# Optimization experiments

Hardware: AMD Instinct MI355X
Metric: run time of the kernel (lower is better)

The kernel has to match this reference:

```python
import jax, jax.numpy as jnp
import numpy as np

C = 512
G = 2  # num_groups in Normalize default
EPS = 1e-6


def setup_inputs() -> dict:
    key = jax.random.key(0)
    ks = jax.random.split(key, 11)
    B, H, W = 4, 64, 64
    s = 1.0 / np.sqrt(C)
    return {
        "x": jax.random.normal(ks[0], (B, C, H, W), dtype=jnp.float32),
        "gn_w": jnp.ones((C,), jnp.float32),
        "gn_b": jnp.zeros((C,), jnp.float32),
        "wq": jax.random.normal(ks[1], (C, C), jnp.float32) * s,
        "bq": jnp.zeros((C,), jnp.float32),
        "wk": jax.random.normal(ks[2], (C, C), jnp.float32) * s,
        "bk": jnp.zeros((C,), jnp.float32),
        "wv": jax.random.normal(ks[3], (C, C), jnp.float32) * s,
        "bv": jnp.zeros((C,), jnp.float32),
        "wp": jax.random.normal(ks[4], (C, C), jnp.float32) * s,
        "bp": jnp.zeros((C,), jnp.float32),
    }


def _group_norm(x, w, b):
    # x: [B, C, H, W]; GroupNorm over (C//G, H, W) within each group
    B, Cc, H, Wd = x.shape
    xg = x.reshape(B, G, Cc // G, H, Wd)
    mu = jnp.mean(xg, axis=(2, 3, 4), keepdims=True)
    var = jnp.var(xg, axis=(2, 3, 4), keepdims=True)
    xn = (xg - mu) * jax.lax.rsqrt(var + EPS)
    xn = xn.reshape(B, Cc, H, Wd)
    return xn * w[None, :, None, None] + b[None, :, None, None]


def _conv1x1(x, w, b):
    # 1x1 conv == channel matmul. x: [B,C,H,W], w: [O,C]
    return jnp.einsum('bchw,oc->bohw', x, w) + b[None, :, None, None]


def reference(x, gn_w, gn_b, wq, bq, wk, bk, wv, bv, wp, bp):
    B, Cc, H, Wd = x.shape
    h_ = _group_norm(x, gn_w, gn_b)
    q = _conv1x1(h_, wq, bq).reshape(B, Cc, H * Wd)  # [B,C,N]
    k = _conv1x1(h_, wk, bk).reshape(B, Cc, H * Wd)
    v = _conv1x1(h_, wv, bv).reshape(B, Cc, H * Wd)
    # scores: q^T k, scaled by sqrt(C) (NOTE: faithful to source, which
    # multiplies by c**0.5 instead of dividing)
    scale = jnp.sqrt(jnp.float32(Cc)).astype(x.dtype)
    attn = jnp.einsum('bcn,bcm->bnm', q, k) * scale  # [B,N,N]
    attn = jax.nn.softmax(attn, axis=2)
    # h_[b,c,n] = sum_m attn[b,n,m] * v[b,c,m]
    out = jnp.einsum('bnm,bcm->bcn', attn, v).reshape(B, Cc, H, Wd)
    out = _conv1x1(out, wp, bp)
    return x + out
```

## Files before the change

### kernel.cpp

```cpp
#include <hip/hip_runtime.h>
#include <hip/hip_bf16.h>
#include <math.h>

#define B_ 4
#define C_ 512
#define N_ 4096

typedef float f32x4 __attribute__((ext_vector_type(4)));
typedef __bf16 bf16x8 __attribute__((ext_vector_type(8)));

#define AS1(p) ((const __attribute__((address_space(1))) unsigned int*)(p))
#define AS3(p) ((__attribute__((address_space(3))) unsigned int*)(p))

__device__ __forceinline__ unsigned short f2bf(float x){
    return __builtin_bit_cast(unsigned short, (__bf16)x);
}
__device__ __forceinline__ float bf2f(unsigned short b){
    unsigned u = ((unsigned)b)<<16;
    return __builtin_bit_cast(float, u);
}
__device__ __forceinline__ f32x4 mfma16(bf16x8 a, bf16x8 b, f32x4 c){
    return __builtin_amdgcn_mfma_f32_16x16x32_bf16(a, b, c, 0, 0, 0);
}

__global__ void split_w(const float* __restrict__ src, unsigned short* __restrict__ hi,
                        unsigned short* __restrict__ lo){
    const int i = (blockIdx.x*256 + threadIdx.x)*4;
    f32x4 v = *(const f32x4*)(src + i);
    ushort4 h, l;
    unsigned short t0=f2bf(v[0]); h.x=t0; l.x=f2bf(v[0]-bf2f(t0));
    unsigned short t1=f2bf(v[1]); h.y=t1; l.y=f2bf(v[1]-bf2f(t1));
    unsigned short t2=f2bf(v[2]); h.z=t2; l.z=f2bf(v[2]-bf2f(t2));
    unsigned short t3=f2bf(v[3]); h.w=t3; l.w=f2bf(v[3]-bf2f(t3));
    *(ushort4*)(hi + i) = h;
    *(ushort4*)(lo + i) = l;
}

__global__ void gn_part(const float* __restrict__ x, float2* __restrict__ part){
    const int bg = blockIdx.y, blk = blockIdx.x, t = threadIdx.x;
    const float* base = x + (size_t)bg*(256*4096) + (size_t)blk*16384;
    float s = 0.f, q = 0.f;
    for (int i=0;i<16;i++){
        f32x4 v = *(const f32x4*)(base + i*1024 + t*4);
        s += v[0]+v[1]+v[2]+v[3];
        q += v[0]*v[0]+v[1]*v[1]+v[2]*v[2]+v[3]*v[3];
    }
    #pragma unroll
    for (int o=32;o>0;o>>=1){ s += __shfl_down(s, o); q += __shfl_down(q, o); }
    __shared__ float as[4], aq[4];
    if ((t&63)==0){ as[t>>6]=s; aq[t>>6]=q; }
    __syncthreads();
    if (t==0)
        part[bg*64 + blk] = make_float2(as[0]+as[1]+as[2]+as[3], aq[0]+aq[1]+aq[2]+aq[3]);
}

__global__ void gn_fin(const float2* __restrict__ part, float2* __restrict__ stats){
    const int bg = blockIdx.x, t = threadIdx.x;
    float2 p = part[bg*64 + t];
    float s = p.x, q = p.y;
    #pragma unroll
    for (int o=32;o>0;o>>=1){ s += __shfl_down(s,o); q += __shfl_down(q,o); }
    if (t==0){
        const float inv = 1.0f/(256.f*4096.f);
        float mu = s*inv;
        float var = q*inv - mu*mu;
        stats[bg] = make_float2(mu, rsqrtf(var + 1e-6f));
    }
}

__global__ void gn_apply(const float* __restrict__ x, const float* __restrict__ gw,
                         const float* __restrict__ gb, const float2* __restrict__ stats,
                         unsigned short* __restrict__ hTh, unsigned short* __restrict__ hTl)
{
    const int b = blockIdx.z, c0 = blockIdx.y*32, n0 = blockIdx.x*32;
    const int t = threadIdx.x;
    __shared__ float tile[32][37];
    {
        const int cl = t>>3, nl = (t&7)*4;
        const int c = c0 + cl;
        const float2 st = stats[b*2 + (c>>8)];
        const float wv = gw[c], bvv = gb[c];
        const f32x4 v = *(const f32x4*)(x + ((size_t)b*C_ + c)*N_ + n0 + nl);
        #pragma unroll
        for (int i=0;i<4;i++) tile[cl][nl+i] = (v[i] - st.x)*st.y*wv + bvv;
    }
    __syncthreads();
    {
        const int nl = t>>3, cl = (t&7)*4;
        const int n = n0 + nl;
        float f0 = tile[cl+0][nl], f1 = tile[cl+1][nl], f2 = tile[cl+2][nl], f3 = tile[cl+3][nl];
        unsigned short h0=f2bf(f0), h1=f2bf(f1), h2=f2bf(f2), h3=f2bf(f3);
        ushort4 hh, ll;
        hh.x=h0; hh.y=h1; hh.z=h2; hh.w=h3;
        ll.x=f2bf(f0-bf2f(h0)); ll.y=f2bf(f1-bf2f(h1));
        ll.z=f2bf(f2-bf2f(h2)); ll.w=f2bf(f3-bf2f(h3));
        size_t o = ((size_t)b*N_ + n)*C_ + c0 + cl;
        *(ushort4*)(hTh + o) = hh;
        *(ushort4*)(hTl + o) = ll;
    }
}

template<int PROD, int MODE>
__global__ __launch_bounds__(256, 2) void conv_gemm(
    const unsigned short* __restrict__ Wh, const unsigned short* __restrict__ Wl,
    const unsigned short* __restrict__ Sh, const unsigned short* __restrict__ Sl,
    const float* __restrict__ bias,
    unsigned short* __restrict__ outHi, unsigned short* __restrict__ outLo,
    float* __restrict__ outF, const float* __restrict__ resid)
{
    const int b = blockIdx.z, o0 = blockIdx.y*128, n0 = blockIdx.x*128;
    const int t = threadIdx.x, w = t>>6, l = t&63, lr = l&15, lg = l>>4;
    const int ro = (w>>1)*64, co = (w&1)*64;
    __shared__ unsigned short Ah[128][40];
    __shared__ unsigned short Al[128][40];
    __shared__ unsigned short Bh[128][40];
    __shared__ unsigned short Bl[128][40];
    f32x4 acc[4][4];
    #pragma unroll
    for (int i=0;i<4;i++)
        #pragma unroll
        for (int j=0;j<4;j++) acc[i][j] = (f32x4){0.f,0.f,0.f,0.f};

    const size_t srcB = (size_t)b*N_*C_;
    for (int ks=0; ks<16; ks++){
        const int c0 = ks*32;
        #pragma unroll
        for (int i=0;i<2;i++){
            int u = t + i*256;
            int row = u>>2, sch = (u&3)*8;
            *(bf16x8*)&Ah[row][sch] = *(const bf16x8*)(Wh + (size_t)(o0+row)*C_ + c0 + sch);
            *(bf16x8*)&Bh[row][sch] = *(const bf16x8*)(Sh + srcB + (size_t)(n0+row)*C_ + c0 + sch);
            if constexpr (PROD==3){
                *(bf16x8*)&Al[row][sch] = *(const bf16x8*)(Wl + (size_t)(o0+row)*C_ + c0 + sch);
                *(bf16x8*)&Bl[row][sch] = *(const bf16x8*)(Sl + srcB + (size_t)(n0+row)*C_ + c0 + sch);
            }
        }
        __syncthreads();
        bf16x8 af[4], bfv[4], afl[4], bfl[4];
        #pragma unroll
        for (int i=0;i<4;i++){
            af[i]  = *(const bf16x8*)&Ah[ro + i*16 + lr][lg*8];
            bfv[i] = *(const bf16x8*)&Bh[co + i*16 + lr][lg*8];
            if constexpr (PROD==3){
                afl[i] = *(const bf16x8*)&Al[ro + i*16 + lr][lg*8];
                bfl[i] = *(const bf16x8*)&Bl[co + i*16 + lr][lg*8];
            }
        }
        #pragma unroll
        for (int i=0;i<4;i++)
            #pragma unroll
            for (int j=0;j<4;j++){
                acc[i][j] = mfma16(af[i], bfv[j], acc[i][j]);
                if constexpr (PROD==3){
                    acc[i][j] = mfma16(af[i],  bfl[j], acc[i][j]);
                    acc[i][j] = mfma16(afl[i], bfv[j], acc[i][j]);
                }
            }
        __syncthreads();
    }
    #pragma unroll
    for (int i=0;i<4;i++){
        const int ob = o0 + ro + i*16 + lg*4;
        #pragma unroll
        for (int j=0;j<4;j++){
            const int n = n0 + co + j*16 + lr;
            f32x4 v = acc[i][j];
            if constexpr (MODE==0){
                float v0 = v[0] + bias[ob+0]; unsigned short h0 = f2bf(v0);
                float v1 = v[1] + bias[ob+1]; unsigned short h1 = f2bf(v1);
                float v2 = v[2] + bias[ob+2]; unsigned short h2 = f2bf(v2);
                float v3 = v[3] + bias[ob+3]; unsigned short h3 = f2bf(v3);
                ushort4 hh, ll;
                hh.x=h0; hh.y=h1; hh.z=h2; hh.w=h3;
                ll.x=f2bf(v0-bf2f(h0)); ll.y=f2bf(v1-bf2f(h1));
                ll.z=f2bf(v2-bf2f(h2)); ll.w=f2bf(v3-bf2f(h3));
                *(ushort4*)(outHi + srcB + (size_t)n*C_ + ob) = hh;
                *(ushort4*)(outLo + srcB + (size_t)n*C_ + ob) = ll;
            } else if constexpr (MODE==1){
                #pragma unroll
                for (int r=0;r<4;r++)
                    outHi[((size_t)b*C_ + ob + r)*N_ + n] = f2bf(v[r] + bias[ob+r]);
            } else {
                #pragma unroll
                for (int r=0;r<4;r++){
                    size_t idx = ((size_t)b*C_ + ob + r)*N_ + n;
                    outF[idx] = resid[idx] + v[r] + bias[ob+r];
                }
            }
        }
    }
}

__global__ __launch_bounds__(512, 2) void attn_flash4(
    const unsigned short* __restrict__ qTh, const unsigned short* __restrict__ qTl,
    const unsigned short* __restrict__ kTh, const unsigned short* __restrict__ kTl,
    const unsigned short* __restrict__ vB,  unsigned short* __restrict__ aoT)
{
    const int id = blockIdx.x;
    const int xcd = id & 7, slot = id >> 3;
    const int b = xcd >> 1;
    const int n0 = ((xcd & 1)*32 + slot)*64;
    const int t = threadIdx.x, w = t>>6, l = t&63, lr = l&15, lg = l>>4;
    const int fm2 = w>>2, fn = (w>>1)&1, ch = w&1;
    const int cw = w*64;

    __shared__ unsigned short khA[32*512];
    __shared__ unsigned short klA[32*512];
    __shared__ unsigned short khB[32*512];
    __shared__ unsigned short klB[32*512];
    __shared__ float Sb[2][64][33];
    __shared__ __align__(16) unsigned short Pb[64*32];
    __shared__ float rowM[64], rowS[64], rowF[64];

    bf16x8 qh[2][8], ql[2][8];
    #pragma unroll
    for (int f=0; f<2; f++){
        const size_t qr = ((size_t)b*N_ + n0 + fm2*32 + f*16 + lr)*C_ + ch*256;
        #pragma unroll
        for (int kc=0; kc<8; kc++){
            qh[f][kc] = *(const bf16x8*)(qTh + qr + kc*32 + lg*8);
            ql[f][kc] = *(const bf16x8*)(qTl + qr + kc*32 + lg*8);
        }
    }
    f32x4 accO[4][4];
    #pragma unroll
    for (int i=0;i<4;i++)
        #pragma unroll
        for (int j=0;j<4;j++) accO[i][j] = (f32x4){0.f,0.f,0.f,0.f};
    if (t < 64){ rowM[t] = -INFINITY; rowS[t] = 0.f; }

    const size_t kBase = (size_t)b*N_*1024;

    auto stage = [&](int mt, unsigned short* dh, unsigned short* dl){
        const size_t kb = kBase + (size_t)mt*32*1024;
        #pragma unroll
        for (int i=0;i<4;i++){
            const int d = i*8192 + t*16;
            const int row = i*8 + w;
            const int colb = (l*16) ^ ((row&7)<<4);
            const size_t g = kb + (size_t)row*1024 + colb;
            __builtin_amdgcn_global_load_lds(AS1((const char*)kTh + g), AS3((char*)dh + d), 16, 0, 0);
            __builtin_amdgcn_global_load_lds(AS1((const char*)kTl + g), AS3((char*)dl + d), 16, 0, 0);
        }
    };
    auto loadV = [&](int mt, bf16x8* vf){
        const size_t vcol = (size_t)mt*32 + lg*8;
        #pragma unroll
        for (int ac=0;ac<4;ac++)
            vf[ac] = *(const bf16x8*)(vB + ((size_t)b*C_ + cw + ac*16 + lr)*N_ + vcol);
    };
    const float SC = 22.62741699796952f;
    auto qk_tile = [&](const unsigned short* kh, const unsigned short* kl){
        f32x4 s0 = (f32x4){0.f,0.f,0.f,0.f}, s1 = s0;
        const int krow = fn*16 + lr;
        const int rbase = krow*1024;
        const int swz = (krow&7)<<4;
        #pragma unroll
        for (int kc=0;kc<8;kc++){
            const int o = rbase + ((ch*512 + kc*64 + lg*16) ^ swz);
            bf16x8 kf  = *(const bf16x8*)((const char*)kh + o);
            bf16x8 kfl = *(const bf16x8*)((const char*)kl + o);
            s0 = mfma16(qh[0][kc], kf,  s0);
            s0 = mfma16(ql[0][kc], kf,  s0);
            s0 = mfma16(qh[0][kc], kfl, s0);
            s1 = mfma16(qh[1][kc], kf,  s1);
            s1 = mfma16(ql[1][kc], kf,  s1);
            s1 = mfma16(qh[1][kc], kfl, s1);
        }
        #pragma unroll
        for (int r=0;r<4;r++){
            Sb[ch][fm2*32 +      lg*4 + r][fn*16 + lr] = s0[r]*SC;
            Sb[ch][fm2*32 + 16 + lg*4 + r][fn*16 + lr] = s1[r]*SC;
        }
    };

    bf16x8 vf[4];
    loadV(0, vf);
    stage(0, khA, klA);
    asm volatile("s_waitcnt vmcnt(0) lgkmcnt(0)" ::: "memory");
    __builtin_amdgcn_s_barrier();
    stage(1, khB, klB);
    qk_tile(khA, klA);
    asm volatile("s_waitcnt lgkmcnt(0)" ::: "memory");
    __builtin_amdgcn_s_barrier();

    for (int mt=0; mt<128; mt++){
        {
            const int row = t>>3, j = t&7;
            const float* s0p = &Sb[0][row][j*4];
            const float* s1p = &Sb[1][row][j*4];
            float a0 = s0p[0] + s1p[0];
            float a1 = s0p[1] + s1p[1];
            float a2 = s0p[2] + s1p[2];
            float a3 = s0p[3] + s1p[3];
            float mx = fmaxf(fmaxf(a0,a1), fmaxf(a2,a3));
            mx = fmaxf(mx, __shfl_xor(mx, 1, 8));
            mx = fmaxf(mx, __shfl_xor(mx, 2, 8));
            mx = fmaxf(mx, __shfl_xor(mx, 4, 8));
            const float mprev = rowM[row];
            const float mnew = fmaxf(mprev, mx);
            float p0 = __expf(a0 - mnew), p1 = __expf(a1 - mnew);
            float p2 = __expf(a2 - mnew), p3 = __expf(a3 - mnew);
            float ps = (p0+p1)+(p2+p3);
            ps += __shfl_xor(ps, 1, 8);
            ps += __shfl_xor(ps, 2, 8);
            ps += __shfl_xor(ps, 4, 8);
            ushort4 pk; pk.x=f2bf(p0); pk.y=f2bf(p1); pk.z=f2bf(p2); pk.w=f2bf(p3);
            char* pw = (char*)Pb + row*64 + ((((j>>1) + (row>>1)) & 3)<<4) + ((j&1)<<3);
            *(ushort4*)pw = pk;
            if (j==0){
                float f = __expf(mprev - mnew);
                rowF[row] = f;
                rowS[row] = rowS[row]*f + ps;
                rowM[row] = mnew;
            }
        }
        asm volatile("s_waitcnt vmcnt(0) lgkmcnt(0)" ::: "memory");
        __builtin_amdgcn_s_barrier();

        if (mt < 126) stage(mt+2, (mt&1) ? khB : khA, (mt&1) ? klB : klA);
        __builtin_amdgcn_s_setprio(1);
        {
            float frv[4][4]; bool need = false;
            #pragma unroll
            for (int am=0;am<4;am++)
                #pragma unroll
                for (int r=0;r<4;r++){
                    frv[am][r] = rowF[am*16 + lg*4 + r];
                    need |= (frv[am][r] != 1.0f);
                }
            if (__any(need)){
                #pragma unroll
                for (int am=0;am<4;am++)
                    #pragma unroll
                    for (int ac=0;ac<4;ac++)
                        #pragma unroll
                        for (int r=0;r<4;r++) accO[am][ac][r] *= frv[am][r];
            }
            bf16x8 pa[4];
            #pragma unroll
            for (int am=0;am<4;am++){
                const int prow = am*16 + lr;
                pa[am] = *(const bf16x8*)((const char*)Pb + prow*64 + (((lg + (prow>>1)) & 3)<<4));
            }
            #pragma unroll
            for (int ac=0;ac<4;ac++)
                #pragma unroll
                for (int am=0;am<4;am++)
                    accO[am][ac] = mfma16(pa[am], vf[ac], accO[am][ac]);
        }
        if (mt < 127){
            loadV(mt+1, vf);
            qk_tile(((mt+1)&1) ? khB : khA, ((mt+1)&1) ? klB : klA);
        }
        __builtin_amdgcn_s_setprio(0);
        asm volatile("s_waitcnt lgkmcnt(0)" ::: "memory");
        __builtin_amdgcn_s_barrier();
    }

    #pragma unroll
    for (int am=0;am<4;am++)
        #pragma unroll
        for (int r=0;r<4;r++){
            const int n = am*16 + lg*4 + r;
            const float inv = 1.0f / rowS[n];
            #pragma unroll
            for (int ac=0;ac<4;ac++)
                aoT[((size_t)b*N_ + n0 + n)*C_ + cw + ac*16 + lr] = f2bf(accO[am][ac][r]*inv);
        }
}

extern "C" void kernel_launch(void* const* d_in, const int* in_sizes, int n_in,
                              void* d_out, int out_size, void* d_ws, size_t ws_size,
                              hipStream_t stream)
{
    const float* x   = (const float*)d_in[0];
    const float* gnw = (const float*)d_in[1];
    const float* gnb = (const float*)d_in[2];
    const float* wq  = (const float*)d_in[3];
    const float* bq  = (const float*)d_in[4];
    const float* wk  = (const float*)d_in[5];
    const float* bk  = (const float*)d_in[6];
    const float* wv  = (const float*)d_in[7];
    const float* bv  = (const float*)d_in[8];
    const float* wp  = (const float*)d_in[9];
    const float* bp  = (const float*)d_in[10];
    float* out = (float*)d_out;

    char* ws = (char*)d_ws;
    size_t off = 0;
    auto alloc = [&](size_t bytes)->char*{
        char* p = ws + off; off += (bytes + 255) & ~(size_t)255; return p;
    };
    const size_t WB = (size_t)C_*C_*2;
    const size_t TB = (size_t)B_*N_*C_*2;
    unsigned short* wqh = (unsigned short*)alloc(WB);
    unsigned short* wql = (unsigned short*)alloc(WB);
    unsigned short* wkh = (unsigned short*)alloc(WB);
    unsigned short* wkl = (unsigned short*)alloc(WB);
    unsigned short* wvh = (unsigned short*)alloc(WB);
    unsigned short* wvl = (unsigned short*)alloc(WB);
    unsigned short* wph = (unsigned short*)alloc(WB);
    unsigned short* wpl = (unsigned short*)alloc(WB);
    unsigned short* hTh = (unsigned short*)alloc(TB);
    unsigned short* hTl = (unsigned short*)alloc(TB);
    unsigned short* qTh = (unsigned short*)alloc(TB);
    unsigned short* qTl = (unsigned short*)alloc(TB);
    unsigned short* kTh = (unsigned short*)alloc(TB);
    unsigned short* kTl = (unsigned short*)alloc(TB);
    unsigned short* vb  = (unsigned short*)alloc(TB);
    unsigned short* ao  = (unsigned short*)alloc(TB);
    float2* part  = (float2*)alloc(8*64*sizeof(float2));
    float2* stats = (float2*)alloc(8*sizeof(float2));

    split_w<<<256, 256, 0, stream>>>(wq, wqh, wql);
    split_w<<<256, 256, 0, stream>>>(wk, wkh, wkl);
    split_w<<<256, 256, 0, stream>>>(wv, wvh, wvl);
    split_w<<<256, 256, 0, stream>>>(wp, wph, wpl);
    gn_part<<<dim3(64, 8), 256, 0, stream>>>(x, part);
    gn_fin<<<8, 64, 0, stream>>>(part, stats);
    gn_apply<<<dim3(128, 16, B_), 256, 0, stream>>>(x, gnw, gnb, stats, hTh, hTl);
    conv_gemm<3,0><<<dim3(32,4,B_), 256, 0, stream>>>(wqh,wql,hTh,hTl,bq, qTh,qTl,nullptr,nullptr);
    conv_gemm<3,0><<<dim3(32,4,B_), 256, 0, stream>>>(wkh,wkl,hTh,hTl,bk, kTh,kTl,nullptr,nullptr);
    conv_gemm<1,1><<<dim3(32,4,B_), 256, 0, stream>>>(wvh,wvl,hTh,hTl,bv, vb,nullptr,nullptr,nullptr);
    attn_flash4<<<dim3(256), 512, 0, stream>>>(qTh,qTl,kTh,kTl,vb,ao);
    conv_gemm<1,2><<<dim3(32,4,B_), 256, 0, stream>>>(wph,wpl,ao,nullptr,bp, nullptr,nullptr,out,x);
}
```

Measured before the change: 494.9 us.

## Software-pipeline flash attention loop to one barrier per tile with double-buffered scores

Restructures the attention main loop into a skewed pipeline where QK for tile t+1, softmax for tile t and PV for tile t-1 run in one iteration with a single barrier, using double-buffered score, probability and rescale-factor buffers. The two channel-half partial scores are now combined with LDS atomicAdd into a swizzled, padded buffer. Softmax reads it as a vector and zeroes it for reuse, replacing the separate per-half arrays. The intent is to remove one barrier per tile and let V loads stay in flight across the barrier via a partial vmcnt wait. The cost is LDS atomics and extra shared memory.

New measurement: 1.126 ms. 2.28x slower.

```diff
diff --git a/kernel.cpp b/kernel.cpp
--- a/kernel.cpp
+++ b/kernel.cpp
@@ -191,7 +191,7 @@
     }
 }
 
-__global__ __launch_bounds__(512, 2) void attn_flash4(
+__global__ __launch_bounds__(512, 2) void attn_flash5(
     const unsigned short* __restrict__ qTh, const unsigned short* __restrict__ qTl,
     const unsigned short* __restrict__ kTh, const unsigned short* __restrict__ kTl,
     const unsigned short* __restrict__ vB,  unsigned short* __restrict__ aoT)
@@ -208,9 +208,9 @@
     __shared__ unsigned short klA[32*512];
     __shared__ unsigned short khB[32*512];
     __shared__ unsigned short klB[32*512];
-    __shared__ float Sb[2][64][33];
-    __shared__ __align__(16) unsigned short Pb[64*32];
-    __shared__ float rowM[64], rowS[64], rowF[64];
+    __shared__ float Sb[2][64][36];
+    __shared__ __align__(16) unsigned short Pb[2][64*32];
+    __shared__ float rowM[64], rowS[64], rowF[2][64];
 
     bf16x8 qh[2][8], ql[2][8];
     #pragma unroll
@@ -227,6 +227,8 @@
     for (int i=0;i<4;i++)
         #pragma unroll
         for (int j=0;j<4;j++) accO[i][j] = (f32x4){0.f,0.f,0.f,0.f};
+
+    for (int i = t; i < 2*64*36; i += 512) ((float*)Sb)[i] = 0.f;
     if (t < 64){ rowM[t] = -INFINITY; rowS[t] = 0.f; }
 
     const size_t kBase = (size_t)b*N_*1024;
@@ -243,56 +245,58 @@
             __builtin_amdgcn_global_load_lds(AS1((const char*)kTl + g), AS3((char*)dl + d), 16, 0, 0);
         }
     };
-    auto loadV = [&](int mt, bf16x8* vf){
-        const size_t vcol = (size_t)mt*32 + lg*8;
-        #pragma unroll
-        for (int ac=0;ac<4;ac++)
-            vf[ac] = *(const bf16x8*)(vB + ((size_t)b*C_ + cw + ac*16 + lr)*N_ + vcol);
-    };
     const float SC = 22.62741699796952f;
-    auto qk_tile = [&](const unsigned short* kh, const unsigned short* kl){
-        f32x4 s0 = (f32x4){0.f,0.f,0.f,0.f}, s1 = s0;
-        const int krow = fn*16 + lr;
-        const int rbase = krow*1024;
-        const int swz = (krow&7)<<4;
-        #pragma unroll
-        for (int kc=0;kc<8;kc++){
-            const int o = rbase + ((ch*512 + kc*64 + lg*16) ^ swz);
-            bf16x8 kf  = *(const bf16x8*)((const char*)kh + o);
-            bf16x8 kfl = *(const bf16x8*)((const char*)kl + o);
-            s0 = mfma16(qh[0][kc], kf,  s0);
-            s0 = mfma16(ql[0][kc], kf,  s0);
-            s0 = mfma16(qh[0][kc], kfl, s0);
-            s1 = mfma16(qh[1][kc], kf,  s1);
-            s1 = mfma16(ql[1][kc], kf,  s1);
-            s1 = mfma16(qh[1][kc], kfl, s1);
-        }
-        #pragma unroll
-        for (int r=0;r<4;r++){
-            Sb[ch][fm2*32 +      lg*4 + r][fn*16 + lr] = s0[r]*SC;
-            Sb[ch][fm2*32 + 16 + lg*4 + r][fn*16 + lr] = s1[r]*SC;
-        }
-    };
-
-    bf16x8 vf[4];
-    loadV(0, vf);
+
     stage(0, khA, klA);
     asm volatile("s_waitcnt vmcnt(0) lgkmcnt(0)" ::: "memory");
     __builtin_amdgcn_s_barrier();
-    stage(1, khB, klB);
-    qk_tile(khA, klA);
-    asm volatile("s_waitcnt lgkmcnt(0)" ::: "memory");
-    __builtin_amdgcn_s_barrier();
-
-    for (int mt=0; mt<128; mt++){
-        {
+
+    bf16x8 vf[4];
+
+    for (int tt = -1; tt <= 128; ++tt){
+        if (tt <= 125)
+            stage(tt+2, ((tt+2)&1) ? khB : khA, ((tt+2)&1) ? klB : klA);
+
+        if (tt <= 126){
+            const unsigned short* kh = ((tt+1)&1) ? khB : khA;
+            const unsigned short* kl = ((tt+1)&1) ? klB : klA;
+            f32x4 s0 = (f32x4){0.f,0.f,0.f,0.f}, s1 = s0;
+            const int krow = fn*16 + lr;
+            const int rbase = krow*1024;
+            const int swz = (krow&7)<<4;
+            __builtin_amdgcn_s_setprio(1);
+            #pragma unroll
+            for (int kc=0;kc<8;kc++){
+                const int o = rbase + ((ch*512 + kc*64 + lg*16) ^ swz);
+                bf16x8 kf  = *(const bf16x8*)((const char*)kh + o);
+                bf16x8 kfl = *(const bf16x8*)((const char*)kl + o);
+                s0 = mfma16(qh[0][kc], kf,  s0);
+                s0 = mfma16(ql[0][kc], kf,  s0);
+                s0 = mfma16(qh[0][kc], kfl, s0);
+                s1 = mfma16(qh[1][kc], kf,  s1);
+                s1 = mfma16(ql[1][kc], kf,  s1);
+                s1 = mfma16(qh[1][kc], kfl, s1);
+            }
+            __builtin_amdgcn_s_setprio(0);
+            float* sb = &Sb[(tt+1)&1][0][0];
+            const int colL = fn*16 + lr;
+            #pragma unroll
+            for (int r=0;r<4;r++){
+                const int row0 = fm2*32 + lg*4 + r;
+                const int col0 = colL ^ ((((row0>>1)&7))<<2);
+                atomicAdd(&sb[row0*36 + col0], s0[r]*SC);
+                atomicAdd(&sb[(row0+16)*36 + col0], s1[r]*SC);
+            }
+        }
+
+        if (tt >= 0 && tt <= 127){
+            float* sbuf = &Sb[tt&1][0][0];
             const int row = t>>3, j = t&7;
-            const float* s0p = &Sb[0][row][j*4];
-            const float* s1p = &Sb[1][row][j*4];
-            float a0 = s0p[0] + s1p[0];
-            float a1 = s0p[1] + s1p[1];
-            float a2 = s0p[2] + s1p[2];
-            float a3 = s0p[3] + s1p[3];
+            float* srow = sbuf + row*36;
+            const int cs = (4*j) ^ ((((row>>1)&7))<<2);
+            f32x4 a4 = *(f32x4*)(srow + cs);
+            *(f32x4*)(srow + cs) = (f32x4){0.f,0.f,0.f,0.f};
+            float a0=a4[0], a1=a4[1], a2=a4[2], a3=a4[3];
             float mx = fmaxf(fmaxf(a0,a1), fmaxf(a2,a3));
             mx = fmaxf(mx, __shfl_xor(mx, 1, 8));
             mx = fmaxf(mx, __shfl_xor(mx, 2, 8));
@@ -306,27 +310,24 @@
             ps += __shfl_xor(ps, 2, 8);
             ps += __shfl_xor(ps, 4, 8);
             ushort4 pk; pk.x=f2bf(p0); pk.y=f2bf(p1); pk.z=f2bf(p2); pk.w=f2bf(p3);
-            char* pw = (char*)Pb + row*64 + ((((j>>1) + (row>>1)) & 3)<<4) + ((j&1)<<3);
+            char* pw = (char*)&Pb[tt&1][0] + row*64 + ((((j>>1) + (row>>1)) & 3)<<4) + ((j&1)<<3);
             *(ushort4*)pw = pk;
             if (j==0){
                 float f = __expf(mprev - mnew);
-                rowF[row] = f;
+                rowF[tt&1][row] = f;
                 rowS[row] = rowS[row]*f + ps;
                 rowM[row] = mnew;
             }
         }
-        asm volatile("s_waitcnt vmcnt(0) lgkmcnt(0)" ::: "memory");
-        __builtin_amdgcn_s_barrier();
-
-        if (mt < 126) stage(mt+2, (mt&1) ? khB : khA, (mt&1) ? klB : klA);
-        __builtin_amdgcn_s_setprio(1);
-        {
+
+        if (tt >= 1){
+            const float* rf = rowF[(tt-1)&1];
             float frv[4][4]; bool need = false;
             #pragma unroll
             for (int am=0;am<4;am++)
                 #pragma unroll
                 for (int r=0;r<4;r++){
-                    frv[am][r] = rowF[am*16 + lg*4 + r];
+                    frv[am][r] = rf[am*16 + lg*4 + r];
                     need |= (frv[am][r] != 1.0f);
                 }
             if (__any(need)){
@@ -337,24 +338,33 @@
                         #pragma unroll
                         for (int r=0;r<4;r++) accO[am][ac][r] *= frv[am][r];
             }
+            const char* pbuf = (const char*)&Pb[(tt-1)&1][0];
             bf16x8 pa[4];
             #pragma unroll
             for (int am=0;am<4;am++){
                 const int prow = am*16 + lr;
-                pa[am] = *(const bf16x8*)((const char*)Pb + prow*64 + (((lg + (prow>>1)) & 3)<<4));
-            }
+                pa[am] = *(const bf16x8*)(pbuf + prow*64 + (((lg + (prow>>1)) & 3)<<4));
+            }
+            __builtin_amdgcn_s_setprio(1);
             #pragma unroll
             for (int ac=0;ac<4;ac++)
                 #pragma unroll
                 for (int am=0;am<4;am++)
                     accO[am][ac] = mfma16(pa[am], vf[ac], accO[am][ac]);
-        }
-        if (mt < 127){
-            loadV(mt+1, vf);
-            qk_tile(((mt+1)&1) ? khB : khA, ((mt+1)&1) ? klB : klA);
-        }
-        __builtin_amdgcn_s_setprio(0);
-        asm volatile("s_waitcnt lgkmcnt(0)" ::: "memory");
+            __builtin_amdgcn_s_setprio(0);
+        }
+
+        if (tt >= 0 && tt <= 127){
+            const size_t vcol = (size_t)tt*32 + lg*8;
+            #pragma unroll
+            for (int ac=0;ac<4;ac++)
+                vf[ac] = *(const bf16x8*)(vB + ((size_t)b*C_ + cw + ac*16 + lr)*N_ + vcol);
+        }
+
+        if (tt >= 0 && tt <= 127)
+            asm volatile("s_waitcnt vmcnt(4) lgkmcnt(0)" ::: "memory");
+        else
+            asm volatile("s_waitcnt vmcnt(0) lgkmcnt(0)" ::: "memory");
         __builtin_amdgcn_s_barrier();
     }
 
@@ -423,6 +433,6 @@
     conv_gemm<3,0><<<dim3(32,4,B_), 256, 0, stream>>>(wqh,wql,hTh,hTl,bq, qTh,qTl,nullptr,nullptr);
     conv_gemm<3,0><<<dim3(32,4,B_), 256, 0, stream>>>(wkh,wkl,hTh,hTl,bk, kTh,kTl,nullptr,nullptr);
     conv_gemm<1,1><<<dim3(32,4,B_), 256, 0, stream>>>(wvh,wvl,hTh,hTl,bv, vb,nullptr,nullptr,nullptr);
-    attn_flash4<<<dim3(256), 512, 0, stream>>>(qTh,qTl,kTh,kTl,vb,ao);
+    attn_flash5<<<dim3(256), 512, 0, stream>>>(qTh,qTl,kTh,kTl,vb,ao);
     conv_gemm<1,2><<<dim3(32,4,B_), 256, 0, stream>>>(wph,wpl,ao,nullptr,bp, nullptr,nullptr,out,x);
 }
```

## Software-pipeline PV matmul one tile behind softmax with double-buffered P

Applied to the files above, without the earlier changes.

Restructures the flash-attention loop so the P·V MFMA for tile it-1 runs at the top of iteration it, before the softmax for tile it, using double-buffered P and rescale-factor arrays. A single barrier per iteration then separates the softmax from the next QK tile and K staging. Both K tiles are prefetched up front with a partial vmcnt wait. Setprio is moved to wrap only the MFMA sections. The P buffer drops its XOR swizzle for padded rows, which may bring back LDS bank conflicts. LDS use also grows slightly, which may affect the 2-blocks-per-CU occupancy.

After: 533.5 us. 7.8% more time.

```diff
diff --git a/kernel.cpp b/kernel.cpp
--- a/kernel.cpp
+++ b/kernel.cpp
@@ -191,7 +191,7 @@
     }
 }
 
-__global__ __launch_bounds__(512, 2) void attn_flash4(
+__global__ __launch_bounds__(512, 2) void attn_flash6(
     const unsigned short* __restrict__ qTh, const unsigned short* __restrict__ qTl,
     const unsigned short* __restrict__ kTh, const unsigned short* __restrict__ kTl,
     const unsigned short* __restrict__ vB,  unsigned short* __restrict__ aoT)
@@ -208,9 +208,9 @@
     __shared__ unsigned short klA[32*512];
     __shared__ unsigned short khB[32*512];
     __shared__ unsigned short klB[32*512];
-    __shared__ float Sb[2][64][33];
-    __shared__ __align__(16) unsigned short Pb[64*32];
-    __shared__ float rowM[64], rowS[64], rowF[64];
+    __shared__ float Sb[2][64][34];
+    __shared__ __align__(16) unsigned short Pb[2][64][34];
+    __shared__ float rowM[64], rowS[64], rowF[2][64];
 
     bf16x8 qh[2][8], ql[2][8];
     #pragma unroll
@@ -255,6 +255,7 @@
         const int krow = fn*16 + lr;
         const int rbase = krow*1024;
         const int swz = (krow&7)<<4;
+        __builtin_amdgcn_s_setprio(1);
         #pragma unroll
         for (int kc=0;kc<8;kc++){
             const int o = rbase + ((ch*512 + kc*64 + lg*16) ^ swz);
@@ -267,6 +268,7 @@
             s1 = mfma16(ql[1][kc], kf,  s1);
             s1 = mfma16(qh[1][kc], kfl, s1);
         }
+        __builtin_amdgcn_s_setprio(0);
         #pragma unroll
         for (int r=0;r<4;r++){
             Sb[ch][fm2*32 +      lg*4 + r][fn*16 + lr] = s0[r]*SC;
@@ -275,16 +277,44 @@
     };
 
     bf16x8 vf[4];
-    loadV(0, vf);
+
     stage(0, khA, klA);
-    asm volatile("s_waitcnt vmcnt(0) lgkmcnt(0)" ::: "memory");
+    stage(1, khB, klB);
+    asm volatile("s_waitcnt vmcnt(8)" ::: "memory");
     __builtin_amdgcn_s_barrier();
-    stage(1, khB, klB);
     qk_tile(khA, klA);
     asm volatile("s_waitcnt lgkmcnt(0)" ::: "memory");
     __builtin_amdgcn_s_barrier();
 
-    for (int mt=0; mt<128; mt++){
+    for (int it=0; it<128; ++it){
+        if (it > 0){
+            const int pp = (it-1)&1;
+            float frv[4][4]; bool need = false;
+            #pragma unroll
+            for (int am=0;am<4;am++)
+                #pragma unroll
+                for (int r=0;r<4;r++){
+                    frv[am][r] = rowF[pp][am*16 + lg*4 + r];
+                    need |= (frv[am][r] != 1.0f);
+                }
+            if (__any(need)){
+                #pragma unroll
+                for (int am=0;am<4;am++)
+                    #pragma unroll
+                    for (int ac=0;ac<4;ac++)
+                        #pragma unroll
+                        for (int r=0;r<4;r++) accO[am][ac][r] *= frv[am][r];
+            }
+            __builtin_amdgcn_s_setprio(1);
+            #pragma unroll
+            for (int am=0;am<4;am++){
+                bf16x8 pa = *(const bf16x8*)&Pb[pp][am*16 + lr][lg*8];
+                #pragma unroll
+                for (int ac=0;ac<4;ac++)
+                    accO[am][ac] = mfma16(pa, vf[ac], accO[am][ac]);
+            }
+            __builtin_amdgcn_s_setprio(0);
+        }
         {
             const int row = t>>3, j = t&7;
             const float* s0p = &Sb[0][row][j*4];
@@ -306,11 +336,10 @@
             ps += __shfl_xor(ps, 2, 8);
             ps += __shfl_xor(ps, 4, 8);
             ushort4 pk; pk.x=f2bf(p0); pk.y=f2bf(p1); pk.z=f2bf(p2); pk.w=f2bf(p3);
-            char* pw = (char*)Pb + row*64 + ((((j>>1) + (row>>1)) & 3)<<4) + ((j&1)<<3);
-            *(ushort4*)pw = pk;
+            *(ushort4*)&Pb[it&1][row][j*4] = pk;
             if (j==0){
                 float f = __expf(mprev - mnew);
-                rowF[row] = f;
+                rowF[it&1][row] = f;
                 rowS[row] = rowS[row]*f + ps;
                 rowM[row] = mnew;
             }
@@ -318,44 +347,38 @@
         asm volatile("s_waitcnt vmcnt(0) lgkmcnt(0)" ::: "memory");
         __builtin_amdgcn_s_barrier();
 
-        if (mt < 126) stage(mt+2, (mt&1) ? khB : khA, (mt&1) ? klB : klA);
-        __builtin_amdgcn_s_setprio(1);
-        {
-            float frv[4][4]; bool need = false;
-            #pragma unroll
-            for (int am=0;am<4;am++)
-                #pragma unroll
-                for (int r=0;r<4;r++){
-                    frv[am][r] = rowF[am*16 + lg*4 + r];
-                    need |= (frv[am][r] != 1.0f);
-                }
-            if (__any(need)){
-                #pragma unroll
-                for (int am=0;am<4;am++)
-                    #pragma unroll
-                    for (int ac=0;ac<4;ac++)
-                        #pragma unroll
-                        for (int r=0;r<4;r++) accO[am][ac][r] *= frv[am][r];
-            }
-            bf16x8 pa[4];
-            #pragma unroll
-            for (int am=0;am<4;am++){
-                const int prow = am*16 + lr;
-                pa[am] = *(const bf16x8*)((const char*)Pb + prow*64 + (((lg + (prow>>1)) & 3)<<4));
-            }
-            #pragma unroll
-            for (int ac=0;ac<4;ac++)
-                #pragma unroll
-                for (int am=0;am<4;am++)
-                    accO[am][ac] = mfma16(pa[am], vf[ac], accO[am][ac]);
-        }
-        if (mt < 127){
-            loadV(mt+1, vf);
-            qk_tile(((mt+1)&1) ? khB : khA, ((mt+1)&1) ? klB : klA);
-        }
-        __builtin_amdgcn_s_setprio(0);
+        if (it <= 125) stage(it+2, (it&1) ? khB : khA, (it&1) ? klB : klA);
+        loadV(it, vf);
+        if (it <= 126) qk_tile(((it+1)&1) ? khB : khA, ((it+1)&1) ? klB : klA);
         asm volatile("s_waitcnt lgkmcnt(0)" ::: "memory");
         __builtin_amdgcn_s_barrier();
+    }
+
+    {
+        const int pp = 1;
+        float frv[4][4]; bool need = false;
+        #pragma unroll
+        for (int am=0;am<4;am++)
+            #pragma unroll
+            for (int r=0;r<4;r++){
+                frv[am][r] = rowF[pp][am*16 + lg*4 + r];
+                need |= (frv[am][r] != 1.0f);
+            }
+        if (__any(need)){
+            #pragma unroll
+            for (int am=0;am<4;am++)
+                #pragma unroll
+                for (int ac=0;ac<4;ac++)
+                    #pragma unroll
+                    for (int r=0;r<4;r++) accO[am][ac][r] *= frv[am][r];
+        }
+        #pragma unroll
+        for (int am=0;am<4;am++){
+            bf16x8 pa = *(const bf16x8*)&Pb[pp][am*16 + lr][lg*8];
+            #pragma unroll
+            for (int ac=0;ac<4;ac++)
+                accO[am][ac] = mfma16(pa, vf[ac], accO[am][ac]);
+        }
     }
 
     #pragma unroll
@@ -423,6 +446,6 @@
     conv_gemm<3,0><<<dim3(32,4,B_), 256, 0, stream>>>(wqh,wql,hTh,hTl,bq, qTh,qTl,nullptr,nullptr);
     conv_gemm<3,0><<<dim3(32,4,B_), 256, 0, stream>>>(wkh,wkl,hTh,hTl,bk, kTh,kTl,nullptr,nullptr);
     conv_gemm<1,1><<<dim3(32,4,B_), 256, 0, stream>>>(wvh,wvl,hTh,hTl,bv, vb,nullptr,nullptr,nullptr);
-    attn_flash4<<<dim3(256), 512, 0, stream>>>(qTh,qTl,kTh,kTl,vb,ao);
+    attn_flash6<<<dim3(256), 512, 0, stream>>>(qTh,qTl,kTh,kTl,vb,ao);
     conv_gemm<1,2><<<dim3(32,4,B_), 256, 0, stream>>>(wph,wpl,ao,nullptr,bp, nullptr,nullptr,out,x);
 }
```

## Warp-specialize flash attention into QK producer and PV consumer waves

Applied to the files above, without the earlier changes.

Rewrites the attention kernel so four waves compute Q·K^T scores with 32x32x16 MFMAs while the other four do the softmax and P·V, handing scores across through a shared-memory buffer. Only the K-high half is staged into LDS; K-low and V are read straight from global memory. Softmax now runs per row in registers with exp2 and a folded scale instead of shuffle reductions. The aim is to overlap the score and value matmuls and to use larger MFMA tiles, at the cost of an imbalanced split between the two wave roles and heavier direct global traffic for K-low and V.

Result: slower. 1.079 ms (+118.1%).

```diff
diff --git a/kernel.cpp b/kernel.cpp
--- a/kernel.cpp
+++ b/kernel.cpp
@@ -7,6 +7,7 @@
 #define N_ 4096
 
 typedef float f32x4 __attribute__((ext_vector_type(4)));
+typedef float f32x16 __attribute__((ext_vector_type(16)));
 typedef __bf16 bf16x8 __attribute__((ext_vector_type(8)));
 
 #define AS1(p) ((const __attribute__((address_space(1))) unsigned int*)(p))
@@ -21,6 +22,9 @@
 }
 __device__ __forceinline__ f32x4 mfma16(bf16x8 a, bf16x8 b, f32x4 c){
     return __builtin_amdgcn_mfma_f32_16x16x32_bf16(a, b, c, 0, 0, 0);
+}
+__device__ __forceinline__ f32x16 mfma32(bf16x8 a, bf16x8 b, f32x16 c){
+    return __builtin_amdgcn_mfma_f32_32x32x16_bf16(a, b, c, 0, 0, 0);
 }
 
 __global__ void split_w(const float* __restrict__ src, unsigned short* __restrict__ hi,
@@ -191,7 +195,7 @@
     }
 }
 
-__global__ __launch_bounds__(512, 2) void attn_flash4(
+__global__ __launch_bounds__(512, 2) void attn_flash8(
     const unsigned short* __restrict__ qTh, const unsigned short* __restrict__ qTl,
     const unsigned short* __restrict__ kTh, const unsigned short* __restrict__ kTl,
     const unsigned short* __restrict__ vB,  unsigned short* __restrict__ aoT)
@@ -200,174 +204,200 @@
     const int xcd = id & 7, slot = id >> 3;
     const int b = xcd >> 1;
     const int n0 = ((xcd & 1)*32 + slot)*64;
-    const int t = threadIdx.x, w = t>>6, l = t&63, lr = l&15, lg = l>>4;
-    const int fm2 = w>>2, fn = (w>>1)&1, ch = w&1;
-    const int cw = w*64;
-
-    __shared__ unsigned short khA[32*512];
-    __shared__ unsigned short klA[32*512];
-    __shared__ unsigned short khB[32*512];
-    __shared__ unsigned short klB[32*512];
-    __shared__ float Sb[2][64][33];
-    __shared__ __align__(16) unsigned short Pb[64*32];
-    __shared__ float rowM[64], rowS[64], rowF[64];
-
-    bf16x8 qh[2][8], ql[2][8];
-    #pragma unroll
-    for (int f=0; f<2; f++){
-        const size_t qr = ((size_t)b*N_ + n0 + fm2*32 + f*16 + lr)*C_ + ch*256;
-        #pragma unroll
-        for (int kc=0; kc<8; kc++){
-            qh[f][kc] = *(const bf16x8*)(qTh + qr + kc*32 + lg*8);
-            ql[f][kc] = *(const bf16x8*)(qTl + qr + kc*32 + lg*8);
-        }
-    }
-    f32x4 accO[4][4];
-    #pragma unroll
-    for (int i=0;i<4;i++)
-        #pragma unroll
-        for (int j=0;j<4;j++) accO[i][j] = (f32x4){0.f,0.f,0.f,0.f};
-    if (t < 64){ rowM[t] = -INFINITY; rowS[t] = 0.f; }
+    const int t = threadIdx.x, w = t>>6, l = t&63, l31 = l&31, h = l>>5;
+    const bool isQK = (w < 4);
+    const int nh = isQK ? (w & 1) : ((w-4) & 1);
+    const int ch = (w>>1) & 1;
+    const int cq = (w-4) >> 1;
+
+    __shared__ unsigned short khb[2][32*512];
+    __shared__ __align__(16) float Sb[2][64][36];
+    __shared__ float rowFb[2][32], rowSb[2][32];
+
+    f32x16 st[8];
+
+    auto getq = [&](int s)->bf16x8{
+        f32x4 tv; const int i = s>>2, j = (s&3)*4;
+        tv[0]=st[i][j]; tv[1]=st[i][j+1]; tv[2]=st[i][j+2]; tv[3]=st[i][j+3];
+        return __builtin_bit_cast(bf16x8, tv);
+    };
+    auto setq = [&](int s, bf16x8 v){
+        f32x4 tv = __builtin_bit_cast(f32x4, v);
+        const int i = s>>2, j = (s&3)*4;
+        st[i][j]=tv[0]; st[i][j+1]=tv[1]; st[i][j+2]=tv[2]; st[i][j+3]=tv[3];
+    };
+
+    if (isQK){
+        const size_t qr = ((size_t)b*N_ + n0 + nh*32 + l31)*C_ + ch*256 + h*8;
+        #pragma unroll
+        for (int ks=0; ks<16; ks++){
+            setq(ks,      *(const bf16x8*)(qTh + qr + ks*16));
+            setq(16+ks,   *(const bf16x8*)(qTl + qr + ks*16));
+        }
+    } else {
+        #pragma unroll
+        for (int f=0; f<8; f++) st[f] = (f32x16)0.0f;
+    }
 
     const size_t kBase = (size_t)b*N_*1024;
 
-    auto stage = [&](int mt, unsigned short* dh, unsigned short* dl){
-        const size_t kb = kBase + (size_t)mt*32*1024;
-        #pragma unroll
-        for (int i=0;i<4;i++){
-            const int d = i*8192 + t*16;
-            const int row = i*8 + w;
+    auto stage = [&](int mt, int bi){
+        const size_t kb = kBase + (size_t)mt*32768;
+        #pragma unroll
+        for (int i=0;i<8;i++){
+            const int row = w*8 + i;
             const int colb = (l*16) ^ ((row&7)<<4);
-            const size_t g = kb + (size_t)row*1024 + colb;
-            __builtin_amdgcn_global_load_lds(AS1((const char*)kTh + g), AS3((char*)dh + d), 16, 0, 0);
-            __builtin_amdgcn_global_load_lds(AS1((const char*)kTl + g), AS3((char*)dl + d), 16, 0, 0);
-        }
-    };
-    auto loadV = [&](int mt, bf16x8* vf){
-        const size_t vcol = (size_t)mt*32 + lg*8;
-        #pragma unroll
-        for (int ac=0;ac<4;ac++)
-            vf[ac] = *(const bf16x8*)(vB + ((size_t)b*C_ + cw + ac*16 + lr)*N_ + vcol);
-    };
-    const float SC = 22.62741699796952f;
-    auto qk_tile = [&](const unsigned short* kh, const unsigned short* kl){
-        f32x4 s0 = (f32x4){0.f,0.f,0.f,0.f}, s1 = s0;
-        const int krow = fn*16 + lr;
-        const int rbase = krow*1024;
-        const int swz = (krow&7)<<4;
-        #pragma unroll
-        for (int kc=0;kc<8;kc++){
-            const int o = rbase + ((ch*512 + kc*64 + lg*16) ^ swz);
-            bf16x8 kf  = *(const bf16x8*)((const char*)kh + o);
-            bf16x8 kfl = *(const bf16x8*)((const char*)kl + o);
-            s0 = mfma16(qh[0][kc], kf,  s0);
-            s0 = mfma16(ql[0][kc], kf,  s0);
-            s0 = mfma16(qh[0][kc], kfl, s0);
-            s1 = mfma16(qh[1][kc], kf,  s1);
-            s1 = mfma16(ql[1][kc], kf,  s1);
-            s1 = mfma16(qh[1][kc], kfl, s1);
-        }
-        #pragma unroll
-        for (int r=0;r<4;r++){
-            Sb[ch][fm2*32 +      lg*4 + r][fn*16 + lr] = s0[r]*SC;
-            Sb[ch][fm2*32 + 16 + lg*4 + r][fn*16 + lr] = s1[r]*SC;
-        }
-    };
-
-    bf16x8 vf[4];
-    loadV(0, vf);
-    stage(0, khA, klA);
-    asm volatile("s_waitcnt vmcnt(0) lgkmcnt(0)" ::: "memory");
+            __builtin_amdgcn_global_load_lds(
+                AS1((const char*)kTh + kb + (size_t)row*1024 + colb),
+                AS3((char*)khb + bi*32768 + row*1024 + l*16), 16, 0, 0);
+        }
+    };
+
+    f32x16 sres;
+    auto qk_compute = [&](int kt){
+        f32x16 s0 = (f32x16)0.0f, s1 = (f32x16)0.0f;
+        const char* khB = (const char*)khb + (kt&1)*32768 + l31*1024;
+        const int swz = (l31&7)<<4;
+        const int cb0 = ch*512 + h*16;
+        const char* klB = (const char*)kTl + kBase + (size_t)(kt*32 + l31)*1024 + cb0;
+        #pragma unroll
+        for (int ks=0; ks<8; ks++){
+            {
+                bf16x8 khf = *(const bf16x8*)(khB + ((cb0 + ks*32) ^ swz));
+                bf16x8 klf = *(const bf16x8*)(klB + ks*32);
+                s0 = mfma32(khf, getq(ks),    s0);
+                s0 = mfma32(khf, getq(16+ks), s0);
+                s0 = mfma32(klf, getq(ks),    s0);
+            }
+            {
+                bf16x8 khf = *(const bf16x8*)(khB + ((cb0 + (ks+8)*32) ^ swz));
+                bf16x8 klf = *(const bf16x8*)(klB + (ks+8)*32);
+                s1 = mfma32(khf, getq(ks+8),  s1);
+                s1 = mfma32(khf, getq(24+ks), s1);
+                s1 = mfma32(klf, getq(ks+8),  s1);
+            }
+        }
+        sres = s0 + s1;
+    };
+    auto write_S = [&](){
+        #pragma unroll
+        for (int q=0;q<4;q++){
+            f32x4 v; v[0]=sres[q*4]; v[1]=sres[q*4+1]; v[2]=sres[q*4+2]; v[3]=sres[q*4+3];
+            *(f32x4*)&Sb[ch][nh*32 + l31][q*8 + h*4] = v;
+        }
+    };
+
+    const float SC2 = 32.6444625f;
+    float m_run = -INFINITY, s_run = 0.f;
+
+    auto pv_iter = [&](int tt){
+        float p[32];
+        const float* s0r = &Sb[0][nh*32 + l31][0];
+        const float* s1r = &Sb[1][nh*32 + l31][0];
+        #pragma unroll
+        for (int u=0;u<8;u++){
+            f32x4 a = *(const f32x4*)(s0r + u*4);
+            f32x4 c = *(const f32x4*)(s1r + u*4);
+            #pragma unroll
+            for (int i=0;i<4;i++) p[u*4+i] = (a[i]+c[i])*SC2;
+        }
+        float m8[16];
+        #pragma unroll
+        for (int i=0;i<16;i++) m8[i] = fmaxf(p[i], p[i+16]);
+        #pragma unroll
+        for (int i=0;i<8;i++)  m8[i] = fmaxf(m8[i], m8[i+8]);
+        #pragma unroll
+        for (int i=0;i<4;i++)  m8[i] = fmaxf(m8[i], m8[i+4]);
+        float mx = fmaxf(fmaxf(m8[0],m8[1]), fmaxf(m8[2],m8[3]));
+        const float mnew = fmaxf(m_run, mx);
+        const float f = exp2f(m_run - mnew);
+        m_run = mnew;
+        #pragma unroll
+        for (int i=0;i<32;i++) p[i] = exp2f(p[i] - mnew);
+        float a8[16];
+        #pragma unroll
+        for (int i=0;i<16;i++) a8[i] = p[i] + p[i+16];
+        #pragma unroll
+        for (int i=0;i<8;i++)  a8[i] += a8[i+8];
+        #pragma unroll
+        for (int i=0;i<4;i++)  a8[i] += a8[i+4];
+        const float ps = (a8[0]+a8[1]) + (a8[2]+a8[3]);
+        s_run = s_run*f + ps;
+        rowFb[nh][l31] = f;
+        float fr[16];
+        #pragma unroll
+        for (int q=0;q<4;q++)
+            #pragma unroll
+            for (int i=0;i<4;i++)
+                fr[q*4+i] = rowFb[nh][i + 8*q + 4*h];
+        bool need = false;
+        #pragma unroll
+        for (int r=0;r<16;r++) need |= (fr[r] != 1.0f);
+        if (__any(need)){
+            #pragma unroll
+            for (int f8=0; f8<8; f8++)
+                #pragma unroll
+                for (int r=0;r<16;r++) st[f8][r] *= fr[r];
+        }
+        bf16x8 pa0, pa1;
+        #pragma unroll
+        for (int j=0;j<8;j++){
+            pa0[j] = (__bf16)p[h*8+j];
+            pa1[j] = (__bf16)p[16+h*8+j];
+        }
+        const size_t vbase = ((size_t)b*C_ + cq*256 + l31)*N_ + tt*32 + h*8;
+        #pragma unroll
+        for (int f8=0; f8<8; f8++){
+            const unsigned short* vp = vB + vbase + (size_t)f8*32*N_;
+            bf16x8 v0 = *(const bf16x8*)(vp);
+            bf16x8 v1 = *(const bf16x8*)(vp + 16);
+            st[f8] = mfma32(pa0, v0, st[f8]);
+            st[f8] = mfma32(pa1, v1, st[f8]);
+        }
+    };
+
+    if (isQK){ stage(0, 0); stage(1, 1); }
+    asm volatile("s_waitcnt vmcnt(0)" ::: "memory");
     __builtin_amdgcn_s_barrier();
-    stage(1, khB, klB);
-    qk_tile(khA, klA);
+    if (isQK) qk_compute(0);
+    __builtin_amdgcn_s_barrier();
+    if (isQK) write_S();
     asm volatile("s_waitcnt lgkmcnt(0)" ::: "memory");
     __builtin_amdgcn_s_barrier();
 
-    for (int mt=0; mt<128; mt++){
-        {
-            const int row = t>>3, j = t&7;
-            const float* s0p = &Sb[0][row][j*4];
-            const float* s1p = &Sb[1][row][j*4];
-            float a0 = s0p[0] + s1p[0];
-            float a1 = s0p[1] + s1p[1];
-            float a2 = s0p[2] + s1p[2];
-            float a3 = s0p[3] + s1p[3];
-            float mx = fmaxf(fmaxf(a0,a1), fmaxf(a2,a3));
-            mx = fmaxf(mx, __shfl_xor(mx, 1, 8));
-            mx = fmaxf(mx, __shfl_xor(mx, 2, 8));
-            mx = fmaxf(mx, __shfl_xor(mx, 4, 8));
-            const float mprev = rowM[row];
-            const float mnew = fmaxf(mprev, mx);
-            float p0 = __expf(a0 - mnew), p1 = __expf(a1 - mnew);
-            float p2 = __expf(a2 - mnew), p3 = __expf(a3 - mnew);
-            float ps = (p0+p1)+(p2+p3);
-            ps += __shfl_xor(ps, 1, 8);
-            ps += __shfl_xor(ps, 2, 8);
-            ps += __shfl_xor(ps, 4, 8);
-            ushort4 pk; pk.x=f2bf(p0); pk.y=f2bf(p1); pk.z=f2bf(p2); pk.w=f2bf(p3);
-            char* pw = (char*)Pb + row*64 + ((((j>>1) + (row>>1)) & 3)<<4) + ((j&1)<<3);
-            *(ushort4*)pw = pk;
-            if (j==0){
-                float f = __expf(mprev - mnew);
-                rowF[row] = f;
-                rowS[row] = rowS[row]*f + ps;
-                rowM[row] = mnew;
-            }
-        }
-        asm volatile("s_waitcnt vmcnt(0) lgkmcnt(0)" ::: "memory");
+    for (int tt=0; tt<128; ++tt){
+        if (isQK){
+            if (tt < 126) stage(tt+2, tt&1);
+            if (tt < 127) qk_compute(tt+1);
+            asm volatile("s_waitcnt vmcnt(0)" ::: "memory");
+        } else {
+            pv_iter(tt);
+        }
         __builtin_amdgcn_s_barrier();
-
-        if (mt < 126) stage(mt+2, (mt&1) ? khB : khA, (mt&1) ? klB : klA);
-        __builtin_amdgcn_s_setprio(1);
-        {
-            float frv[4][4]; bool need = false;
-            #pragma unroll
-            for (int am=0;am<4;am++)
-                #pragma unroll
-                for (int r=0;r<4;r++){
-                    frv[am][r] = rowF[am*16 + lg*4 + r];
-                    need |= (frv[am][r] != 1.0f);
-                }
-            if (__any(need)){
-                #pragma unroll
-                for (int am=0;am<4;am++)
-                    #pragma unroll
-                    for (int ac=0;ac<4;ac++)
-                        #pragma unroll
-                        for (int r=0;r<4;r++) accO[am][ac][r] *= frv[am][r];
-            }
-            bf16x8 pa[4];
-            #pragma unroll
-            for (int am=0;am<4;am++){
-                const int prow = am*16 + lr;
-                pa[am] = *(const bf16x8*)((const char*)Pb + prow*64 + (((lg + (prow>>1)) & 3)<<4));
-            }
-            #pragma unroll
-            for (int ac=0;ac<4;ac++)
-                #pragma unroll
-                for (int am=0;am<4;am++)
-                    accO[am][ac] = mfma16(pa[am], vf[ac], accO[am][ac]);
-        }
-        if (mt < 127){
-            loadV(mt+1, vf);
-            qk_tile(((mt+1)&1) ? khB : khA, ((mt+1)&1) ? klB : klA);
-        }
-        __builtin_amdgcn_s_setprio(0);
+        if (isQK && tt < 127) write_S();
         asm volatile("s_waitcnt lgkmcnt(0)" ::: "memory");
         __builtin_amdgcn_s_barrier();
     }
 
-    #pragma unroll
-    for (int am=0;am<4;am++)
-        #pragma unroll
-        for (int r=0;r<4;r++){
-            const int n = am*16 + lg*4 + r;
-            const float inv = 1.0f / rowS[n];
-            #pragma unroll
-            for (int ac=0;ac<4;ac++)
-                aoT[((size_t)b*N_ + n0 + n)*C_ + cw + ac*16 + lr] = f2bf(accO[am][ac][r]*inv);
-        }
+    if (!isQK){
+        rowSb[nh][l31] = s_run;
+        float inv[16];
+        #pragma unroll
+        for (int q=0;q<4;q++)
+            #pragma unroll
+            for (int i=0;i<4;i++)
+                inv[q*4+i] = 1.0f / rowSb[nh][i + 8*q + 4*h];
+        #pragma unroll
+        for (int f8=0; f8<8; f8++)
+            #pragma unroll
+            for (int q=0;q<4;q++)
+                #pragma unroll
+                for (int i=0;i<4;i++){
+                    const int nrow = i + 8*q + 4*h;
+                    aoT[((size_t)b*N_ + n0 + nh*32 + nrow)*C_ + cq*256 + f8*32 + l31]
+                        = f2bf(st[f8][q*4+i] * inv[q*4+i]);
+                }
+    }
 }
 
 extern "C" void kernel_launch(void* const* d_in, const int* in_sizes, int n_in,
@@ -423,6 +453,6 @@
     conv_gemm<3,0><<<dim3(32,4,B_), 256, 0, stream>>>(wqh,wql,hTh,hTl,bq, qTh,qTl,nullptr,nullptr);
     conv_gemm<3,0><<<dim3(32,4,B_), 256, 0, stream>>>(wkh,wkl,hTh,hTl,bk, kTh,kTl,nullptr,nullptr);
     conv_gemm<1,1><<<dim3(32,4,B_), 256, 0, stream>>>(wvh,wvl,hTh,hTl,bv, vb,nullptr,nullptr,nullptr);
-    attn_flash4<<<dim3(256), 512, 0, stream>>>(qTh,qTl,kTh,kTl,vb,ao);
+    attn_flash8<<<dim3(256), 512, 0, stream>>>(qTh,qTl,kTh,kTl,vb,ao);
     conv_gemm<1,2><<<dim3(32,4,B_), 256, 0, stream>>>(wph,wpl,ao,nullptr,bp, nullptr,nullptr,out,x);
 }
```
